# Optimization experiments

Measured on AMD Instinct MI355X. Metric: run time of the kernel, lower is better.

## Reference

```python
import jax, jax.numpy as jnp
import numpy as np

B, DATA_DIM, Z_DIM, H = 16384, 4096, 512, 400


def _linear_params(key, fan_in, fan_out):
    kw, kb = jax.random.split(key)
    s = 1.0 / np.sqrt(fan_in)
    W = jax.random.uniform(kw, (fan_in, fan_out), jnp.float32, -s, s)
    b = jax.random.uniform(kb, (fan_out,), jnp.float32, -s, s)
    return W, b


def setup_inputs() -> dict:
    key = jax.random.key(0)
    ks = jax.random.split(key, 8)
    x = jax.random.uniform(ks[0], (B, DATA_DIM), jnp.float32)  # data in [0,1]
    eps = jax.random.normal(ks[1], (B, Z_DIM), jnp.float32)    # reparam noise
    W1, b1 = _linear_params(ks[2], DATA_DIM, H)
    W21, b21 = _linear_params(ks[3], H, Z_DIM)
    W22, b22 = _linear_params(ks[4], H, 1)
    W23, b23 = _linear_params(ks[5], H, 1)
    W3, b3 = _linear_params(ks[6], Z_DIM, H)
    W4, b4 = _linear_params(ks[7], H, DATA_DIM)
    return {"x": x, "eps": eps, "W1": W1, "b1": b1, "W21": W21, "b21": b21,
            "W22": W22, "b22": b22, "W23": W23, "b23": b23,
            "W3": W3, "b3": b3, "W4": W4, "b4": b4}


def reference(x, eps, W1, b1, W21, b21, W22, b22, W23, b23, W3, b3, W4, b4):
    # encode
    h1 = jax.nn.relu(x @ W1 + b1)                    # [B, 400]
    mu = h1 @ W21 + b21                              # [B, Z]
    rho = jnp.tanh(h1 @ W22 + b22)                   # [B, 1]
    logs = h1 @ W23 + b23                            # [B, 1]
    # reparameterize: the torch loop builds z_q[:, j] = sum_{i<=j} eps_i * sqrt(exp(logs))
    # (logs is per-row constant), i.e. a cumulative sum of scaled Gaussian noise.
    std = jnp.sqrt(jnp.exp(logs))                    # [B, 1]
    z = jnp.cumsum(eps * std, axis=1) + mu           # [B, Z]
    # decode
    h3 = jax.nn.relu(z @ W3 + b3)                    # [B, 400]
    recon = jax.nn.sigmoid(h3 @ W4 + b4)             # [B, DATA_DIM]
    return recon, mu, rho, logs
```

## Files before the change

### kernel.cpp

```cpp
#include <hip/hip_runtime.h>
#include <hip/hip_bf16.h>
#include <math.h>


using f16x8 = __attribute__((ext_vector_type(8))) _Float16;
using f32x4 = __attribute__((ext_vector_type(4))) float;

#define TB   16384
#define DDIM 4096
#define ZD   512
#define HP   512
#define HLOG 400

static constexpr size_t MU_OFF   = (size_t)TB * DDIM;
static constexpr size_t RHO_OFF  = MU_OFF + (size_t)TB * ZD;
static constexpr size_t LOGS_OFF = RHO_OFF + TB;

static constexpr size_t O_W1T  = 0;
static constexpr size_t O_W21T = O_W1T  + (size_t)HP * DDIM * 2;
static constexpr size_t O_W3T  = O_W21T + (size_t)HP * HP * 2;
static constexpr size_t O_W4T  = O_W3T  + (size_t)HP * HP * 2;
static constexpr size_t O_H1P  = O_W4T  + (size_t)DDIM * HP * 2;
static constexpr size_t O_ZA   = O_H1P  + (size_t)TB * HP * 2;
static constexpr size_t O_STD  = O_ZA   + (size_t)TB * ZD * 2;

__device__ __forceinline__ void async_load16(const void* g, void* l) {
  __builtin_amdgcn_global_load_lds(
      (const __attribute__((address_space(1))) unsigned int*)g,
      (__attribute__((address_space(3))) unsigned int*)l, 16, 0, 0);
}

__global__ __launch_bounds__(256) void pack_all(
    const float* __restrict__ W1, const float* __restrict__ W21,
    const float* __restrict__ W3, const float* __restrict__ W4,
    _Float16* __restrict__ W1t, _Float16* __restrict__ W21t,
    _Float16* __restrict__ W3t, _Float16* __restrict__ W4t)
{
  __shared__ float T[32][33];
  int bx = blockIdx.x;
  const float* src; _Float16* dst; int R, C, ds, tk;
  if (bx < 2048)      { src = W1;  dst = W1t;  R = 4096; C = 400;  ds = 4096; tk = 128; }
  else if (bx < 2304) { src = W21; dst = W21t; R = 400;  C = 512;  ds = 512;  tk = 16; bx -= 2048; }
  else if (bx < 2560) { src = W3;  dst = W3t;  R = 512;  C = 400;  ds = 512;  tk = 16; bx -= 2304; }
  else                { src = W4;  dst = W4t;  R = 400;  C = 4096; ds = 512;  tk = 16; bx -= 2560; }
  int tki = bx % tk, tni = bx / tk;
  int tid = threadIdx.x;
#pragma unroll
  for (int it = 0; it < 4; ++it) {
    int idx = it * 256 + tid;
    int i = idx >> 5, j = idx & 31;
    int k = tki * 32 + i, n = tni * 32 + j;
    float val = 0.f;
    if (k < R && n < C) val = src[(size_t)k * C + n];
    T[i][j] = val;
  }
  __syncthreads();
#pragma unroll
  for (int it = 0; it < 4; ++it) {
    int idx = it * 256 + tid;
    int i = idx >> 5, j = idx & 31;
    int n = tni * 32 + i, k = tki * 32 + j;
    dst[(size_t)n * ds + k] = (_Float16)T[j][i];
  }
}

template <int AF32, int EPI>
__global__ __launch_bounds__(256, 2) void gemm_k(
    const void* __restrict__ Av, const _Float16* __restrict__ Bt,
    const float* __restrict__ bias, void* __restrict__ Cv,
    int Nlog, int K, int lda, int ldc)
{
  __shared__ _Float16 Bs[128 * 32];
  __shared__ float    As_f[AF32 ? 128 * 32 : 8];
  __shared__ _Float16 As_h[AF32 ? 8 : 128 * 32];

  const int tid  = threadIdx.x;
  const int lane = tid & 63;
  const int wave = tid >> 6;
  const int quad = lane >> 4;
  const int l15  = lane & 15;
  const int wm   = wave >> 1;
  const int wn   = wave & 1;
  const int mBase = blockIdx.y * 128;
  const int nBase = blockIdx.x * 128;

  const float*    Af = (const float*)Av;
  const _Float16* Ah = (const _Float16*)Av;

  f32x4 acc[4][4];
#pragma unroll
  for (int i = 0; i < 4; ++i)
#pragma unroll
    for (int j = 0; j < 4; ++j)
      acc[i][j] = (f32x4){0.f, 0.f, 0.f, 0.f};

  for (int k0 = 0; k0 < K; k0 += 32) {
#pragma unroll
    for (int is = 0; is < 2; ++is) {
      int f = is * 256 + tid;
      int n = f >> 2, p = f & 3;
      int c = p ^ ((n >> 1) & 3);
      async_load16(Bt + (size_t)(nBase + n) * K + k0 + c * 8,
                   &Bs[(is * 256 + wave * 64) * 8]);
    }
    if constexpr (AF32) {
#pragma unroll
      for (int is = 0; is < 4; ++is) {
        int f = is * 256 + tid;
        int m = f >> 3, p = f & 7;
        int c = p ^ (m & 7);
        async_load16(Af + (size_t)(mBase + m) * lda + k0 + c * 4,
                     &As_f[(is * 256 + wave * 64) * 4]);
      }
    } else {
#pragma unroll
      for (int is = 0; is < 2; ++is) {
        int f = is * 256 + tid;
        int m = f >> 2, p = f & 3;
        int c = p ^ ((m >> 1) & 3);
        async_load16(Ah + (size_t)(mBase + m) * lda + k0 + c * 8,
                     &As_h[(is * 256 + wave * 64) * 8]);
      }
    }
    __builtin_amdgcn_s_waitcnt(0x0f70);
    __syncthreads();

    f16x8 a[4], b[4];
#pragma unroll
    for (int t = 0; t < 4; ++t) {
      int n = wn * 64 + t * 16 + l15;
      b[t] = *(const f16x8*)&Bs[n * 32 + ((quad ^ ((n >> 1) & 3)) * 8)];
    }
    if constexpr (AF32) {
#pragma unroll
      for (int t = 0; t < 4; ++t) {
        int m = wm * 64 + t * 16 + l15;
        int p0 = (2 * quad) ^ (m & 7);
        f32x4 u = *(const f32x4*)&As_f[m * 32 + p0 * 4];
        f32x4 v = *(const f32x4*)&As_f[m * 32 + (p0 ^ 1) * 4];
        f16x8 av;
        av[0] = (_Float16)u[0]; av[1] = (_Float16)u[1];
        av[2] = (_Float16)u[2]; av[3] = (_Float16)u[3];
        av[4] = (_Float16)v[0]; av[5] = (_Float16)v[1];
        av[6] = (_Float16)v[2]; av[7] = (_Float16)v[3];
        a[t] = av;
      }
    } else {
#pragma unroll
      for (int t = 0; t < 4; ++t) {
        int m = wm * 64 + t * 16 + l15;
        a[t] = *(const f16x8*)&As_h[m * 32 + ((quad ^ ((m >> 1) & 3)) * 8)];
      }
    }
#pragma unroll
    for (int i = 0; i < 4; ++i)
#pragma unroll
      for (int j = 0; j < 4; ++j)
        acc[i][j] = __builtin_amdgcn_mfma_f32_16x16x32_f16(a[i], b[j], acc[i][j], 0, 0, 0);
    __syncthreads();
  }

#pragma unroll
  for (int j = 0; j < 4; ++j) {
    int col = nBase + wn * 64 + j * 16 + l15;
    bool cv = col < Nlog;
    float bv = cv ? bias[col] : 0.f;
#pragma unroll
    for (int i = 0; i < 4; ++i) {
      int row0 = mBase + wm * 64 + i * 16 + quad * 4;
#pragma unroll
      for (int r = 0; r < 4; ++r) {
        float v = acc[i][j][r] + bv;
        size_t idx = (size_t)(row0 + r) * ldc + col;
        if constexpr (EPI == 0) {
          v = cv ? fmaxf(v, 0.f) : 0.f;
          ((_Float16*)Cv)[idx] = (_Float16)v;
        } else if constexpr (EPI == 1) {
          ((float*)Cv)[idx] = v;
        } else {
          ((float*)Cv)[idx] = 1.f / (1.f + __expf(-v));
        }
      }
    }
  }
}

__global__ __launch_bounds__(256) void head_k(
    const _Float16* __restrict__ h1p,
    const float* __restrict__ w22, const float* __restrict__ b22,
    const float* __restrict__ w23, const float* __restrict__ b23,
    float* __restrict__ rho, float* __restrict__ logs, float* __restrict__ stdb)
{
  int lane = threadIdx.x & 63;
  int row  = blockIdx.x * 4 + (threadIdx.x >> 6);
  int kk = lane * 8;
  float s22 = 0.f, s23 = 0.f;
  if (kk < HLOG) {
    f16x8 h = *(const f16x8*)&h1p[(size_t)row * HP + kk];
    f32x4 wa = *(const f32x4*)&w22[kk];
    f32x4 wb = *(const f32x4*)&w22[kk + 4];
    f32x4 va = *(const f32x4*)&w23[kk];
    f32x4 vb = *(const f32x4*)&w23[kk + 4];
#pragma unroll
    for (int j = 0; j < 4; ++j) {
      float hv = (float)h[j];
      s22 += hv * wa[j]; s23 += hv * va[j];
    }
#pragma unroll
    for (int j = 0; j < 4; ++j) {
      float hv = (float)h[4 + j];
      s22 += hv * wb[j]; s23 += hv * vb[j];
    }
  }
#pragma unroll
  for (int d = 32; d > 0; d >>= 1) {
    s22 += __shfl_xor(s22, d);
    s23 += __shfl_xor(s23, d);
  }
  if (lane == 0) {
    rho[row] = tanhf(s22 + b22[0]);
    float lg = s23 + b23[0];
    logs[row] = lg;
    stdb[row] = expf(0.5f * lg);
  }
}

__global__ __launch_bounds__(256) void zscan_k(
    const float* __restrict__ eps, const float* __restrict__ mu,
    const float* __restrict__ stdb, _Float16* __restrict__ zA)
{
  int lane = threadIdx.x & 63;
  int row  = blockIdx.x * 4 + (threadIdx.x >> 6);
  int j0 = lane * 8;
  float s = stdb[row];
  const float* er = eps + (size_t)row * ZD + j0;
  f32x4 e0 = *(const f32x4*)er;
  f32x4 e1 = *(const f32x4*)(er + 4);
  float v[8];
  v[0] = e0[0] * s;
  v[1] = v[0] + e0[1] * s;
  v[2] = v[1] + e0[2] * s;
  v[3] = v[2] + e0[3] * s;
  v[4] = v[3] + e1[0] * s;
  v[5] = v[4] + e1[1] * s;
  v[6] = v[5] + e1[2] * s;
  v[7] = v[6] + e1[3] * s;
  float tot = v[7];
  float inc = tot;
#pragma unroll
  for (int d = 1; d < 64; d <<= 1) {
    float t = __shfl_up(inc, d);
    if (lane >= d) inc += t;
  }
  float off = inc - tot;
  const float* mr = mu + (size_t)row * ZD + j0;
  f32x4 m0 = *(const f32x4*)mr;
  f32x4 m1 = *(const f32x4*)(mr + 4);
  f16x8 zv;
#pragma unroll
  for (int j = 0; j < 8; ++j) {
    float mv = (j < 4) ? m0[j] : m1[j - 4];
    zv[j] = (_Float16)(off + v[j] + mv);
  }
  *(f16x8*)&zA[(size_t)row * ZD + j0] = zv;
}

extern "C" void kernel_launch(void* const* d_in, const int* in_sizes, int n_in,
                              void* d_out, int out_size, void* d_ws, size_t ws_size,
                              hipStream_t stream) {
  (void)in_sizes; (void)n_in; (void)out_size; (void)ws_size;
  const float* x   = (const float*)d_in[0];
  const float* eps = (const float*)d_in[1];
  const float* W1  = (const float*)d_in[2];
  const float* b1  = (const float*)d_in[3];
  const float* W21 = (const float*)d_in[4];
  const float* b21 = (const float*)d_in[5];
  const float* W22 = (const float*)d_in[6];
  const float* b22 = (const float*)d_in[7];
  const float* W23 = (const float*)d_in[8];
  const float* b23 = (const float*)d_in[9];
  const float* W3  = (const float*)d_in[10];
  const float* b3  = (const float*)d_in[11];
  const float* W4  = (const float*)d_in[12];
  const float* b4  = (const float*)d_in[13];
  float* out = (float*)d_out;
  char*  ws  = (char*)d_ws;

  _Float16* W1t  = (_Float16*)(ws + O_W1T);
  _Float16* W21t = (_Float16*)(ws + O_W21T);
  _Float16* W3t  = (_Float16*)(ws + O_W3T);
  _Float16* W4t  = (_Float16*)(ws + O_W4T);
  _Float16* h1p  = (_Float16*)(ws + O_H1P);
  _Float16* zA   = (_Float16*)(ws + O_ZA);
  float*    stdb = (float*)(ws + O_STD);
  _Float16* h3p  = h1p;

  pack_all<<<4608, 256, 0, stream>>>(W1, W21, W3, W4, W1t, W21t, W3t, W4t);
  gemm_k<1, 0><<<dim3(4, 128), 256, 0, stream>>>(x, W1t, b1, h1p, HLOG, DDIM, DDIM, HP);
  head_k<<<4096, 256, 0, stream>>>(h1p, W22, b22, W23, b23,
                                   out + RHO_OFF, out + LOGS_OFF, stdb);
  gemm_k<0, 1><<<dim3(4, 128), 256, 0, stream>>>(h1p, W21t, b21, out + MU_OFF, ZD, HP, HP, ZD);
  zscan_k<<<4096, 256, 0, stream>>>(eps, out + MU_OFF, stdb, zA);
  gemm_k<0, 0><<<dim3(4, 128), 256, 0, stream>>>(zA, W3t, b3, h3p, HLOG, ZD, ZD, HP);
  gemm_k<0, 2><<<dim3(32, 128), 256, 0, stream>>>(h3p, W4t, b4, out, DDIM, HP, HP, DDIM);
}
```

Before: 807.6 us.

## Double-buffer GEMM LDS tiles and remap workgroups across XCDs

The GEMM kernel now keeps two LDS buffers for the A and B tiles. It issues the async global-to-LDS loads for the next K-slice before running MFMA on the current slice, so memory latency overlaps with compute. It also remaps the linear workgroup id so that consecutive tiles stay on the same XCD, which is meant to improve L2 reuse. The explicit vmcnt wait was removed, so correctness now relies on the barrier waiting for the outstanding async loads. LDS use doubles, which may limit occupancy.

```diff
diff --git a/kernel.cpp b/kernel.cpp
--- a/kernel.cpp
+++ b/kernel.cpp
@@ -70,9 +70,9 @@
     const float* __restrict__ bias, void* __restrict__ Cv,
     int Nlog, int K, int lda, int ldc)
 {
-  __shared__ _Float16 Bs[128 * 32];
-  __shared__ float    As_f[AF32 ? 128 * 32 : 8];
-  __shared__ _Float16 As_h[AF32 ? 8 : 128 * 32];
+  __shared__ _Float16 Bs[2][128 * 32];
+  __shared__ float    As_f[AF32 ? 2 * 128 * 32 : 8];
+  __shared__ _Float16 As_h[AF32 ? 8 : 2 * 128 * 32];
 
   const int tid  = threadIdx.x;
   const int lane = tid & 63;
@@ -81,8 +81,14 @@
   const int l15  = lane & 15;
   const int wm   = wave >> 1;
   const int wn   = wave & 1;
-  const int mBase = blockIdx.y * 128;
-  const int nBase = blockIdx.x * 128;
+
+  const int gx  = gridDim.x;
+  const int nwg = gx * gridDim.y;
+  const int lb  = blockIdx.y * gx + blockIdx.x;
+  int sb = lb;
+  if ((nwg & 7) == 0) sb = (lb & 7) * (nwg >> 3) + (lb >> 3);
+  const int mBase = (sb / gx) * 128;
+  const int nBase = (sb % gx) * 128;
 
   const float*    Af = (const float*)Av;
   const _Float16* Ah = (const _Float16*)Av;
@@ -94,14 +100,14 @@
     for (int j = 0; j < 4; ++j)
       acc[i][j] = (f32x4){0.f, 0.f, 0.f, 0.f};
 
-  for (int k0 = 0; k0 < K; k0 += 32) {
+  auto stage = [&](int buf, int k0) {
 #pragma unroll
     for (int is = 0; is < 2; ++is) {
       int f = is * 256 + tid;
       int n = f >> 2, p = f & 3;
       int c = p ^ ((n >> 1) & 3);
       async_load16(Bt + (size_t)(nBase + n) * K + k0 + c * 8,
-                   &Bs[(is * 256 + wave * 64) * 8]);
+                   &Bs[buf][(is * 256 + wave * 64) * 8]);
     }
     if constexpr (AF32) {
 #pragma unroll
@@ -110,7 +116,7 @@
         int m = f >> 3, p = f & 7;
         int c = p ^ (m & 7);
         async_load16(Af + (size_t)(mBase + m) * lda + k0 + c * 4,
-                     &As_f[(is * 256 + wave * 64) * 4]);
+                     &As_f[buf * (128 * 32) + (is * 256 + wave * 64) * 4]);
       }
     } else {
 #pragma unroll
@@ -119,25 +125,28 @@
         int m = f >> 2, p = f & 3;
         int c = p ^ ((m >> 1) & 3);
         async_load16(Ah + (size_t)(mBase + m) * lda + k0 + c * 8,
-                     &As_h[(is * 256 + wave * 64) * 8]);
-      }
-    }
-    __builtin_amdgcn_s_waitcnt(0x0f70);
-    __syncthreads();
+                     &As_h[buf * (128 * 32) + (is * 256 + wave * 64) * 8]);
+      }
+    }
+  };
+
+  auto body = [&](int buf, int kk) {
+    if (kk + 32 < K) stage(buf ^ 1, kk + 32);
 
     f16x8 a[4], b[4];
 #pragma unroll
     for (int t = 0; t < 4; ++t) {
       int n = wn * 64 + t * 16 + l15;
-      b[t] = *(const f16x8*)&Bs[n * 32 + ((quad ^ ((n >> 1) & 3)) * 8)];
+      b[t] = *(const f16x8*)&Bs[buf][n * 32 + ((quad ^ ((n >> 1) & 3)) * 8)];
     }
     if constexpr (AF32) {
+      const float* Ab = &As_f[buf * (128 * 32)];
 #pragma unroll
       for (int t = 0; t < 4; ++t) {
         int m = wm * 64 + t * 16 + l15;
         int p0 = (2 * quad) ^ (m & 7);
-        f32x4 u = *(const f32x4*)&As_f[m * 32 + p0 * 4];
-        f32x4 v = *(const f32x4*)&As_f[m * 32 + (p0 ^ 1) * 4];
+        f32x4 u = *(const f32x4*)&Ab[m * 32 + p0 * 4];
+        f32x4 v = *(const f32x4*)&Ab[m * 32 + (p0 ^ 1) * 4];
         f16x8 av;
         av[0] = (_Float16)u[0]; av[1] = (_Float16)u[1];
         av[2] = (_Float16)u[2]; av[3] = (_Float16)u[3];
@@ -146,10 +155,11 @@
         a[t] = av;
       }
     } else {
+      const _Float16* Ab = &As_h[buf * (128 * 32)];
 #pragma unroll
       for (int t = 0; t < 4; ++t) {
         int m = wm * 64 + t * 16 + l15;
-        a[t] = *(const f16x8*)&As_h[m * 32 + ((quad ^ ((m >> 1) & 3)) * 8)];
+        a[t] = *(const f16x8*)&Ab[m * 32 + ((quad ^ ((m >> 1) & 3)) * 8)];
       }
     }
 #pragma unroll
@@ -157,7 +167,16 @@
 #pragma unroll
       for (int j = 0; j < 4; ++j)
         acc[i][j] = __builtin_amdgcn_mfma_f32_16x16x32_f16(a[i], b[j], acc[i][j], 0, 0, 0);
+
     __syncthreads();
+  };
+
+  stage(0, 0);
+  __syncthreads();
+
+  for (int k0 = 0; k0 < K; k0 += 64) {
+    body(0, k0);
+    body(1, k0 + 32);
   }
 
 #pragma unroll
```

After: 768.2 us. 1.05x faster.
